# Kernel tuning notes

Hardware: AMD Instinct MI355X
Metric: run time of the kernel (lower is better)

The kernel has to match this reference:

```python
import jax, jax.numpy as jnp
import numpy as np

B, V, E, K, H = 8, 4096, 256, 6, 8
HD = E // H  # head dim = 32


def _knn_idx(x, k):
    # brute-force squared-euclidean KNN (pytorch3d knn_points, return_sorted=True)
    sq = jnp.sum(x * x, axis=-1)                      # [B, V]
    d2 = sq[:, :, None] + sq[:, None, :] - 2.0 * jnp.einsum('bie,bje->bij', x, x)  # [B,V,V]
    _, idx = jax.lax.top_k(-d2, k)                    # ascending distance -> [B, V, K]
    return idx


def setup_inputs() -> dict:
    key = jax.random.key(0)
    kx, kq, kk, kv, ko = jax.random.split(key, 5)
    s = 1.0 / np.sqrt(E)
    return {
        'x':  jax.random.normal(kx, (B, V, E), dtype=jnp.float32),
        'Wq': jax.random.normal(kq, (E, E), dtype=jnp.float32) * s,
        'Wk': jax.random.normal(kk, (E, E), dtype=jnp.float32) * s,
        'Wv': jax.random.normal(kv, (E, E), dtype=jnp.float32) * s,
        'Wo': jax.random.normal(ko, (E, E), dtype=jnp.float32) * s,
    }


def reference(x, Wq, Wk, Wv, Wo):
    idx = _knn_idx(x, K)                                   # [B, V, K] int32
    k = jax.vmap(lambda xb, ib: xb[ib])(x, idx)            # gather -> [B, V, K, E]
    v = k - x[:, :, None, :]                               # use_direction: v = k - q

    # per-point 1-query / K-key multihead attention (bias-free, eval mode)
    scale = 1.0 / np.sqrt(HD)
    qh = (x @ Wq.T).reshape(B, V, H, HD)                   # [B,V,H,HD]
    kh = jnp.einsum('bvke,fe->bvkf', k, Wk).reshape(B, V, K, H, HD)
    vh = jnp.einsum('bvke,fe->bvkf', v, Wv).reshape(B, V, K, H, HD)
    scores = jnp.einsum('bvhd,bvkhd->bvhk', qh, kh) * scale  # [B,V,H,K]
    attn = jax.nn.softmax(scores, axis=-1)
    out = jnp.einsum('bvhk,bvkhd->bvhd', attn, vh).reshape(B, V, E) @ Wo.T

    # attention weights averaged over heads, scatter-added onto neighbor ids
    x_w = jnp.mean(attn, axis=2)                            # [B, V, K]
    x_w = jax.vmap(lambda i, w: jnp.zeros((V,), x.dtype).at[i].add(w))(
        idx.reshape(B, -1), x_w.reshape(B, -1))             # [B, V]

    return x + out, x_w
```

## Files before the change

### kernel.cpp

```cpp
#include <hip/hip_runtime.h>
#include <cfloat>
#include <math.h>

#define B_   8
#define V_   4096
#define E_   256
#define K_   6
#define H_   8
#define HD_  32
#define NPTS (B_*V_)

typedef __bf16 bf16x8 __attribute__((ext_vector_type(8)));
typedef float  f32x4  __attribute__((ext_vector_type(4)));
typedef float  f32x16 __attribute__((ext_vector_type(16)));

__device__ __forceinline__ float bf2f(unsigned short u) {
    return __uint_as_float(((unsigned int)u) << 16);
}
__device__ __forceinline__ unsigned short f2bf(float f) {
    unsigned int u = __float_as_uint(f);
    return (unsigned short)((u + 0x7fffu + ((u >> 16) & 1u)) >> 16);
}
__device__ __forceinline__ unsigned int med3u(unsigned int a, unsigned int b,
                                              unsigned int c) {
    unsigned int d;
    asm("v_med3_u32 %0, %1, %2, %3" : "=v"(d) : "v"(a), "v"(b), "v"(c));
    return d;
}
__device__ __forceinline__ void push6(unsigned int (&k6)[6], unsigned int key) {
    k6[5] = med3u(k6[4], k6[5], key);
    k6[4] = med3u(k6[3], k6[4], key);
    k6[3] = med3u(k6[2], k6[3], key);
    k6[2] = med3u(k6[1], k6[2], key);
    k6[1] = med3u(k6[0], k6[1], key);
    k6[0] = min(k6[0], key);
}
__device__ __forceinline__ unsigned int bfscale2(unsigned int u) {
    return (u + 0x05000500u) ^ 0x80008000u;
}

__global__ __launch_bounds__(256) void cvtsq_kernel(const float* __restrict__ x,
                                                    const float* __restrict__ Wq,
                                                    const float* __restrict__ Wk,
                                                    const float* __restrict__ Wv,
                                                    const float* __restrict__ Wo,
                                                    unsigned short* __restrict__ xh,
                                                    unsigned short* __restrict__ Wh,
                                                    float* __restrict__ sqp,
                                                    float* __restrict__ xw) {
    const int bx = blockIdx.x;
    if (bx < 4096) {
        size_t i = ((size_t)bx * 256 + threadIdx.x) * 8;
        float4 a = *reinterpret_cast<const float4*>(x + i);
        float4 b = *reinterpret_cast<const float4*>(x + i + 4);
        ushort o[8] = { f2bf(a.x), f2bf(a.y), f2bf(a.z), f2bf(a.w),
                        f2bf(b.x), f2bf(b.y), f2bf(b.z), f2bf(b.w) };
        *reinterpret_cast<uint4*>(xh + i) = *reinterpret_cast<uint4*>(o);
        float s = a.x*a.x + a.y*a.y + a.z*a.z + a.w*a.w
                + b.x*b.x + b.y*b.y + b.z*b.z + b.w*b.w;
        s += __shfl_xor(s, 1);
        s += __shfl_xor(s, 2);
        s += __shfl_xor(s, 4);
        s += __shfl_xor(s, 8);
        s += __shfl_xor(s, 16);
        if ((threadIdx.x & 31) == 0) {
            int p = bx * 8 + (threadIdx.x >> 5);
            int b_ = p >> 12, col = p & 4095;
            int stripe = col >> 10, cc = col & 1023;
            int t = cc >> 5, rem = cc & 31;
            int h = (rem >> 2) & 1;
            int reg = (rem & 3) | ((rem >> 3) << 2);
            int i2 = (b_ << 12) | (stripe << 10) | (t << 5) | (h << 4) | reg;
            sqp[i2] = (s + 600.f) * 512.f;
        }
    } else {
        const int wb = bx - 4096;
        xw[wb * 256 + threadIdx.x] = 0.f;
        const int m = wb >> 5;
        const float* src = (m == 0) ? Wq : (m == 1) ? Wk : (m == 2) ? Wv : Wo;
        unsigned short* dst = Wh + (size_t)m * 65536;
        size_t i = ((size_t)(wb & 31) * 256 + threadIdx.x) * 8;
        float4 a = *reinterpret_cast<const float4*>(src + i);
        float4 b = *reinterpret_cast<const float4*>(src + i + 4);
        ushort o[8] = { f2bf(a.x), f2bf(a.y), f2bf(a.z), f2bf(a.w),
                        f2bf(b.x), f2bf(b.y), f2bf(b.z), f2bf(b.w) };
        *reinterpret_cast<uint4*>(dst + i) = *reinterpret_cast<uint4*>(o);
    }
}

__global__ __launch_bounds__(256, 2) void knn13_kernel(const unsigned short* __restrict__ xh,
                                                       const float* __restrict__ sqp,
                                                       unsigned int* __restrict__ cand) {
    __shared__ __align__(16) char smem[36864];

    const int b      = blockIdx.z;
    const int row0   = blockIdx.x * 256;
    const int stripe = blockIdx.y;
    const int colbase = stripe * 1024;
    const int tid = threadIdx.x;
    const int w   = tid >> 6;
    const int l   = tid & 63;
    const int ln  = l & 31;
    const int h   = l >> 5;
    const unsigned short* Xb = xh + ((size_t)b << 12) * E_;

    const int myrow0 = row0 + (w << 6) + ln;
    bf16x8 brow0[16], brow1[16];
#pragma unroll
    for (int kg = 0; kg < 16; ++kg) {
        uint4 u0 = *reinterpret_cast<const uint4*>(
            Xb + ((size_t)myrow0 << 8) + kg * 16 + h * 8);
        uint4 u1 = *reinterpret_cast<const uint4*>(
            Xb + ((size_t)(myrow0 + 32) << 8) + kg * 16 + h * 8);
        u0.x = bfscale2(u0.x); u0.y = bfscale2(u0.y);
        u0.z = bfscale2(u0.z); u0.w = bfscale2(u0.w);
        u1.x = bfscale2(u1.x); u1.y = bfscale2(u1.y);
        u1.z = bfscale2(u1.z); u1.w = bfscale2(u1.w);
        brow0[kg] = *reinterpret_cast<bf16x8*>(&u0);
        brow1[kg] = *reinterpret_cast<bf16x8*>(&u1);
    }

    unsigned int bk0[6], bk1[6];
#pragma unroll
    for (int s = 0; s < 6; ++s) { bk0[s] = 0xFFFFFFFFu; bk1[s] = 0xFFFFFFFFu; }

    __builtin_amdgcn_global_load_lds(
        (const __attribute__((address_space(1))) void*)
            (sqp + ((size_t)(b * 4 + stripe) << 10) + tid * 4),
        (__attribute__((address_space(3))) void*)(smem + 32768 + tid * 16), 16, 0, 0);
#pragma unroll
    for (int it = 0; it < 4; ++it) {
        int li = it * 256 + tid, col = li >> 5, sl = li & 31;
        const unsigned short* gp =
            Xb + ((size_t)(colbase + col) << 8) + ((sl ^ (col & 7)) << 3);
        __builtin_amdgcn_global_load_lds(
            (const __attribute__((address_space(1))) void*)gp,
            (__attribute__((address_space(3))) void*)(smem + li * 16), 16, 0, 0);
    }
    __syncthreads();

    for (int t = 0; t < 32; ++t) {
        const int cur = (t & 1) * 16384;
        if (t < 31) {
            char* nbuf = smem + (cur ^ 16384);
            const int c0n = colbase + (t + 1) * 32;
#pragma unroll
            for (int it = 0; it < 4; ++it) {
                int li = it * 256 + tid, col = li >> 5, sl = li & 31;
                const unsigned short* gp =
                    Xb + ((size_t)(c0n + col) << 8) + ((sl ^ (col & 7)) << 3);
                __builtin_amdgcn_global_load_lds(
                    (const __attribute__((address_space(1))) void*)gp,
                    (__attribute__((address_space(3))) void*)(nbuf + li * 16), 16, 0, 0);
            }
        }
        const char* sb = smem + 32768 + t * 128 + h * 64;
        f32x16 acc0;
#pragma unroll
        for (int q = 0; q < 4; ++q) {
            f32x4 sv = *reinterpret_cast<const f32x4*>(sb + q * 16);
            acc0[q * 4 + 0] = sv[0];
            acc0[q * 4 + 1] = sv[1];
            acc0[q * 4 + 2] = sv[2];
            acc0[q * 4 + 3] = sv[3];
        }
        f32x16 acc1 = acc0;

        const char* abase = smem + cur + ln * 512;
        const int swz = (ln & 7);
#pragma unroll
        for (int kg = 0; kg < 16; ++kg) {
            bf16x8 af = *reinterpret_cast<const bf16x8*>(
                abase + ((((kg << 1) + h) ^ swz) << 4));
            acc0 = __builtin_amdgcn_mfma_f32_32x32x16_bf16(af, brow0[kg], acc0, 0, 0, 0);
            acc1 = __builtin_amdgcn_mfma_f32_32x32x16_bf16(af, brow1[kg], acc1, 0, 0, 0);
        }

        const unsigned int cb0 = (unsigned int)(colbase + (t << 5) + (h << 2));
#pragma unroll
        for (int r = 0; r < 16; ++r) {
            unsigned int cidx = cb0 + (r & 3) + ((r >> 2) << 3);
            push6(bk0, ((unsigned int)acc0[r] << 12) | cidx);
            push6(bk1, ((unsigned int)acc1[r] << 12) | cidx);
        }
        __syncthreads();
    }

    size_t p0 = ((size_t)b << 12) + myrow0;
    unsigned int* op0 = cand + p0 * 48 + stripe * 12 + h * 6;
    unsigned int* op1 = cand + (p0 + 32) * 48 + stripe * 12 + h * 6;
#pragma unroll
    for (int s = 0; s < 6; ++s) { op0[s] = bk0[s]; op1[s] = bk1[s]; }
}

__global__ __launch_bounds__(256) void sel_kernel(const unsigned int* __restrict__ cand,
                                                  unsigned short* __restrict__ c16,
                                                  int* __restrict__ idxout,
                                                  unsigned char* __restrict__ flag) {
    int p = blockIdx.x * 256 + threadIdx.x;
    const unsigned int* cp = cand + (size_t)p * 48;
    unsigned int tk[16];
#pragma unroll
    for (int s = 0; s < 16; ++s) tk[s] = 0xFFFFFFFFu;
    for (int j = 0; j < 48; ++j) {
        unsigned int key = cp[j];
#pragma unroll
        for (int s = 15; s > 0; --s) tk[s] = med3u(tk[s - 1], tk[s], key);
        tk[0] = min(tk[0], key);
    }
    unsigned short* op = c16 + (size_t)p * 16;
#pragma unroll
    for (int s = 0; s < 16; ++s) op[s] = (unsigned short)(tk[s] & 4095u);
    int* ip = idxout + (size_t)p * K_;
#pragma unroll
    for (int s = 0; s < 6; ++s) ip[s] = (int)(tk[s] & 4095u);
    float d6 = (float)(tk[5] >> 12) * 0.001953125f;
    float d7 = (float)(tk[6] >> 12) * 0.001953125f;
    flag[p] = (d7 - d6 < 0.4f) ? 1 : 0;
}

__global__ __launch_bounds__(256) void refine_kernel(const float* __restrict__ x,
                                                     const unsigned short* __restrict__ c16,
                                                     const unsigned char* __restrict__ flag,
                                                     int* __restrict__ idxout) {
    int wv = threadIdx.x >> 6;
    int lane = threadIdx.x & 63;
    const int bid = blockIdx.x;
    const int nbk = ((bid & 7) << 10) | (bid >> 3);
    int p = nbk * 4 + wv;
    if (!flag[p]) return;
    int b = p >> 12;
    int vi = p & 4095;
    const float* Xb = x + ((size_t)b << 12) * E_;
    const int half = lane >> 5;
    const int hl = lane & 31;

    double xi[8];
#pragma unroll
    for (int t = 0; t < 8; ++t) xi[t] = (double)Xb[(size_t)vi * E_ + hl + t * 32];

    double bdist[6]; int bidx[6];
#pragma unroll
    for (int s = 0; s < 6; ++s) { bdist[s] = DBL_MAX; bidx[s] = 0x7fffffff; }

    const unsigned short* cp = c16 + (size_t)p * 16;
    for (int c = 0; c < 16; c += 2) {
        int jme = cp[c + half];
        const float* Xj = Xb + (size_t)jme * E_;
        double s = 0.0;
#pragma unroll
        for (int t = 0; t < 8; ++t) {
            double d = xi[t] - (double)Xj[hl + t * 32];
            s = fma(d, d, s);
        }
#pragma unroll
        for (int off = 16; off; off >>= 1) s += __shfl_xor(s, off);
        double sv[2];
        sv[0] = __shfl(s, 0);
        sv[1] = __shfl(s, 32);
        int jv[2] = { (int)cp[c], (int)cp[c + 1] };
#pragma unroll
        for (int q = 0; q < 2; ++q) {
            double sq_ = sv[q]; int j = jv[q];
            if (sq_ < bdist[5] || (sq_ == bdist[5] && j < bidx[5])) {
                bdist[5] = sq_; bidx[5] = j;
#pragma unroll
                for (int t = 5; t > 0; --t) {
                    if (bdist[t] < bdist[t - 1] ||
                        (bdist[t] == bdist[t - 1] && bidx[t] < bidx[t - 1])) {
                        double td = bdist[t]; bdist[t] = bdist[t - 1]; bdist[t - 1] = td;
                        int    ti = bidx[t];  bidx[t]  = bidx[t - 1];  bidx[t - 1]  = ti;
                    } else break;
                }
            }
        }
    }
    if (lane == 0) {
        int* op = idxout + (size_t)p * K_;
#pragma unroll
        for (int s = 0; s < 6; ++s) op[s] = bidx[s];
    }
}

__global__ __launch_bounds__(256, 2) void proj_mfma(const unsigned short* __restrict__ xh,
                                                    const unsigned short* __restrict__ Wh,
                                                    unsigned short* __restrict__ Y) {
    const int tid = threadIdx.x;
    const int w = tid >> 6, l = tid & 63, cl = l & 15, g = l >> 4;
    const int row0 = blockIdx.x * 128;
    const int wsel = blockIdx.y;
    const unsigned short* W = Wh + (size_t)wsel * 65536;

    bf16x8 a0[8], a1[8];
    const int ar0 = row0 + (w << 4) + cl;
#pragma unroll
    for (int ks = 0; ks < 8; ++ks) {
        a0[ks] = *reinterpret_cast<const bf16x8*>(xh + ((size_t)ar0 << 8) + ks * 32 + g * 8);
        a1[ks] = *reinterpret_cast<const bf16x8*>(xh + ((size_t)(ar0 + 64) << 8) + ks * 32 + g * 8);
    }

    bf16x8 wf[8];
    {
        const unsigned short* Wr = W + (size_t)cl * 256 + g * 8;
#pragma unroll
        for (int ks = 0; ks < 8; ++ks)
            wf[ks] = *reinterpret_cast<const bf16x8*>(Wr + ks * 32);
    }

#pragma unroll
    for (int ct = 0; ct < 16; ++ct) {
        bf16x8 wn[8];
        if (ct < 15) {
            const unsigned short* Wr = W + (size_t)((ct + 1) * 16 + cl) * 256 + g * 8;
#pragma unroll
            for (int ks = 0; ks < 8; ++ks)
                wn[ks] = *reinterpret_cast<const bf16x8*>(Wr + ks * 32);
        }
        f32x4 acc0 = {0.f, 0.f, 0.f, 0.f};
        f32x4 acc1 = {0.f, 0.f, 0.f, 0.f};
#pragma unroll
        for (int ks = 0; ks < 8; ++ks) {
            acc0 = __builtin_amdgcn_mfma_f32_16x16x32_bf16(a0[ks], wf[ks], acc0, 0, 0, 0);
            acc1 = __builtin_amdgcn_mfma_f32_16x16x32_bf16(a1[ks], wf[ks], acc1, 0, 0, 0);
        }
#pragma unroll
        for (int r = 0; r < 4; ++r) {
            size_t row = row0 + (w << 4) + (g << 2) + r;
            Y[row * 768 + wsel * 256 + ct * 16 + cl] = f2bf(acc0[r]);
            Y[(row + 64) * 768 + wsel * 256 + ct * 16 + cl] = f2bf(acc1[r]);
        }
#pragma unroll
        for (int ks = 0; ks < 8; ++ks) wf[ks] = wn[ks];
    }
}

__global__ __launch_bounds__(256) void attn16_kernel(const unsigned short* __restrict__ Y,
                                                     const int* __restrict__ idx,
                                                     const unsigned short* __restrict__ WoH,
                                                     const float* __restrict__ x,
                                                     float* __restrict__ out,
                                                     float* __restrict__ xw) {
    __shared__ __align__(16) unsigned short P[16][264];
    const int bid = blockIdx.x;
    const int blk = ((bid & 7) << 8) | (bid >> 3);
    const int w = threadIdx.x >> 6;
    const int l = threadIdx.x & 63;
    const int p0 = blk * 16;
    const int b = p0 >> 12;
    const size_t bbase = (size_t)(b << 12) * 768;

    for (int j = 0; j < 4; ++j) {
        const int p = p0 + w * 4 + j;
        const int* ip = idx + (size_t)p * K_;
        int nb[K_];
#pragma unroll
        for (int k = 0; k < K_; ++k) nb[k] = ip[k];

        const unsigned short* Yp = Y + (size_t)p * 768;
        ushort4 q4 = *reinterpret_cast<const ushort4*>(Yp + l * 4);
        ushort4 s4 = *reinterpret_cast<const ushort4*>(Yp + 512 + l * 4);
        float q0 = bf2f(q4.x), q1 = bf2f(q4.y), q2 = bf2f(q4.z), q3 = bf2f(q4.w);
        float v0 = bf2f(s4.x), v1 = bf2f(s4.y), v2 = bf2f(s4.z), v3 = bf2f(s4.w);

        float sc[K_];
#pragma unroll
        for (int k = 0; k < K_; ++k) {
            ushort4 k4 = *reinterpret_cast<const ushort4*>(
                Y + bbase + (size_t)nb[k] * 768 + 256 + l * 4);
            float s = q0 * bf2f(k4.x) + q1 * bf2f(k4.y)
                    + q2 * bf2f(k4.z) + q3 * bf2f(k4.w);
            s += __shfl_xor(s, 1);
            s += __shfl_xor(s, 2);
            s += __shfl_xor(s, 4);
            sc[k] = s * 0.17677669529663687f;
        }
        float m = sc[0];
#pragma unroll
        for (int k = 1; k < K_; ++k) m = fmaxf(m, sc[k]);
        float e[K_], sum = 0.f;
#pragma unroll
        for (int k = 0; k < K_; ++k) { e[k] = __expf(sc[k] - m); sum += e[k]; }
        float inv = 1.f / sum;

        float o0 = 0.f, o1 = 0.f, o2 = 0.f, o3 = 0.f;
        float hs[K_];
#pragma unroll
        for (int k = 0; k < K_; ++k) {
            float a = e[k] * inv;
            ushort4 z4 = *reinterpret_cast<const ushort4*>(
                Y + bbase + (size_t)nb[k] * 768 + 512 + l * 4);
            o0 += a * (bf2f(z4.x) - v0);
            o1 += a * (bf2f(z4.y) - v1);
            o2 += a * (bf2f(z4.z) - v2);
            o3 += a * (bf2f(z4.w) - v3);
            float t = a;
            t += __shfl_xor(t, 8);
            t += __shfl_xor(t, 16);
            t += __shfl_xor(t, 32);
            hs[k] = t * 0.125f;
        }
        ushort o4[4] = { f2bf(o0), f2bf(o1), f2bf(o2), f2bf(o3) };
        *reinterpret_cast<ushort4*>(&P[w * 4 + j][l * 4]) =
            *reinterpret_cast<ushort4*>(o4);
        if (l < K_) atomicAdd(&xw[(b << 12) + nb[l]], hs[l]);
    }
    __syncthreads();

    const int cl = l & 15, g = l >> 4;
    bf16x8 a[8];
#pragma unroll
    for (int ks = 0; ks < 8; ++ks)
        a[ks] = *reinterpret_cast<const bf16x8*>(&P[cl][ks * 32 + g * 8]);

#pragma unroll
    for (int ct = 0; ct < 4; ++ct) {
        const int col0 = w * 64 + ct * 16;
        f32x4 acc = {0.f, 0.f, 0.f, 0.f};
        const unsigned short* Wr = WoH + (size_t)(col0 + cl) * 256 + g * 8;
#pragma unroll
        for (int ks = 0; ks < 8; ++ks) {
            bf16x8 bf = *reinterpret_cast<const bf16x8*>(Wr + ks * 32);
            acc = __builtin_amdgcn_mfma_f32_16x16x32_bf16(a[ks], bf, acc, 0, 0, 0);
        }
#pragma unroll
        for (int r = 0; r < 4; ++r) {
            size_t o = (size_t)(p0 + (g << 2) + r) * E_ + col0 + cl;
            out[o] = acc[r] + x[o];
        }
    }
}

extern "C" void kernel_launch(void* const* d_in, const int* in_sizes, int n_in,
                              void* d_out, int out_size, void* d_ws, size_t ws_size,
                              hipStream_t stream) {
    const float* x  = (const float*)d_in[0];
    const float* Wq = (const float*)d_in[1];
    const float* Wk = (const float*)d_in[2];
    const float* Wv = (const float*)d_in[3];
    const float* Wo = (const float*)d_in[4];

    float* out = (float*)d_out;
    float* xw  = out + (size_t)NPTS * E_;

    char* ws = (char*)d_ws;
    float*          sqpw  = (float*)(ws + 131072);
    unsigned int*   candw = (unsigned int*)(ws + 262144);
    int*            idxw  = (int*)(ws + 6553600);
    unsigned char*  flagw = (unsigned char*)(ws + 7340032);
    unsigned short* Wh    = (unsigned short*)(ws + 7372800);
    unsigned short* c16w  = (unsigned short*)(ws + 7897088);
    unsigned short* Xh    = (unsigned short*)(ws + 8945664);
    unsigned short* Y     = (unsigned short*)(ws + 25722880);

    cvtsq_kernel<<<4096 + 128, 256, 0, stream>>>(x, Wq, Wk, Wv, Wo, Xh, Wh, sqpw, xw);
    knn13_kernel<<<dim3(V_ / 256, 4, B_), 256, 0, stream>>>(Xh, sqpw, candw);
    sel_kernel<<<NPTS / 256, 256, 0, stream>>>(candw, c16w, idxw, flagw);
    refine_kernel<<<NPTS / 4, 256, 0, stream>>>(x, c16w, flagw, idxw);
    proj_mfma<<<dim3(NPTS / 128, 3), 256, 0, stream>>>(Xh, Wh, Y);
    attn16_kernel<<<NPTS / 16, 256, 0, stream>>>(Y, idxw, Wh + 3 * 65536, x, out, xw);
}
```

Baseline: 229.3 us.

## Stage projection weight tiles in LDS via async global_load_lds double buffering

Each wave previously loaded its own copy of the weight tile straight from global memory into registers, so the four waves in a block fetched the same data redundantly. The weights are now loaded once per block into a swizzled, double-buffered LDS tile of 32 output columns using direct global-to-LDS loads, and each wave reads its fragments from LDS. The intent is to cut global and L2 traffic and register pressure in the projection GEMM. In exchange it adds 32KB of LDS per block and a barrier per tile step, which may limit occupancy and serialise the pipeline.

```diff
diff --git a/kernel.cpp b/kernel.cpp
--- a/kernel.cpp
+++ b/kernel.cpp
@@ -285,6 +285,7 @@
 __global__ __launch_bounds__(256, 2) void proj_mfma(const unsigned short* __restrict__ xh,
                                                     const unsigned short* __restrict__ Wh,
                                                     unsigned short* __restrict__ Y) {
+    __shared__ __align__(16) char smem[32768];
     const int tid = threadIdx.x;
     const int w = tid >> 6, l = tid & 63, cl = l & 15, g = l >> 4;
     const int row0 = blockIdx.x * 128;
@@ -299,38 +300,54 @@
         a1[ks] = *reinterpret_cast<const bf16x8*>(xh + ((size_t)(ar0 + 64) << 8) + ks * 32 + g * 8);
     }
 
-    bf16x8 wf[8];
-    {
-        const unsigned short* Wr = W + (size_t)cl * 256 + g * 8;
-#pragma unroll
-        for (int ks = 0; ks < 8; ++ks)
-            wf[ks] = *reinterpret_cast<const bf16x8*>(Wr + ks * 32);
-    }
-
-#pragma unroll
-    for (int ct = 0; ct < 16; ++ct) {
-        bf16x8 wn[8];
-        if (ct < 15) {
-            const unsigned short* Wr = W + (size_t)((ct + 1) * 16 + cl) * 256 + g * 8;
-#pragma unroll
-            for (int ks = 0; ks < 8; ++ks)
-                wn[ks] = *reinterpret_cast<const bf16x8*>(Wr + ks * 32);
-        }
-        f32x4 acc0 = {0.f, 0.f, 0.f, 0.f};
-        f32x4 acc1 = {0.f, 0.f, 0.f, 0.f};
-#pragma unroll
-        for (int ks = 0; ks < 8; ++ks) {
-            acc0 = __builtin_amdgcn_mfma_f32_16x16x32_bf16(a0[ks], wf[ks], acc0, 0, 0, 0);
-            acc1 = __builtin_amdgcn_mfma_f32_16x16x32_bf16(a1[ks], wf[ks], acc1, 0, 0, 0);
-        }
-#pragma unroll
-        for (int r = 0; r < 4; ++r) {
-            size_t row = row0 + (w << 4) + (g << 2) + r;
-            Y[row * 768 + wsel * 256 + ct * 16 + cl] = f2bf(acc0[r]);
-            Y[(row + 64) * 768 + wsel * 256 + ct * 16 + cl] = f2bf(acc1[r]);
-        }
-#pragma unroll
-        for (int ks = 0; ks < 8; ++ks) wf[ks] = wn[ks];
+#pragma unroll
+    for (int it = 0; it < 4; ++it) {
+        int li = it * 256 + tid, col = li >> 5, sl = li & 31;
+        const unsigned short* gp = W + ((size_t)col << 8) + ((sl ^ (col & 7)) << 3);
+        __builtin_amdgcn_global_load_lds(
+            (const __attribute__((address_space(1))) void*)gp,
+            (__attribute__((address_space(3))) void*)(smem + li * 16), 16, 0, 0);
+    }
+    __syncthreads();
+
+    for (int tp = 0; tp < 8; ++tp) {
+        const int cur = (tp & 1) * 16384;
+        if (tp < 7) {
+            char* nbuf = smem + (cur ^ 16384);
+            const int colb = (tp + 1) * 32;
+#pragma unroll
+            for (int it = 0; it < 4; ++it) {
+                int li = it * 256 + tid, col = li >> 5, sl = li & 31;
+                const unsigned short* gp =
+                    W + ((size_t)(colb + col) << 8) + ((sl ^ (col & 7)) << 3);
+                __builtin_amdgcn_global_load_lds(
+                    (const __attribute__((address_space(1))) void*)gp,
+                    (__attribute__((address_space(3))) void*)(nbuf + li * 16), 16, 0, 0);
+            }
+        }
+#pragma unroll
+        for (int c01 = 0; c01 < 2; ++c01) {
+            const int ct = tp * 2 + c01;
+            const int wr = c01 * 16 + cl;
+            const char* wbase = smem + cur + wr * 512;
+            const int swz = wr & 7;
+            f32x4 acc0 = {0.f, 0.f, 0.f, 0.f};
+            f32x4 acc1 = {0.f, 0.f, 0.f, 0.f};
+#pragma unroll
+            for (int ks = 0; ks < 8; ++ks) {
+                bf16x8 wf = *reinterpret_cast<const bf16x8*>(
+                    wbase + ((((ks << 2) + g) ^ swz) << 4));
+                acc0 = __builtin_amdgcn_mfma_f32_16x16x32_bf16(a0[ks], wf, acc0, 0, 0, 0);
+                acc1 = __builtin_amdgcn_mfma_f32_16x16x32_bf16(a1[ks], wf, acc1, 0, 0, 0);
+            }
+#pragma unroll
+            for (int r = 0; r < 4; ++r) {
+                size_t row = row0 + (w << 4) + (g << 2) + r;
+                Y[row * 768 + wsel * 256 + ct * 16 + cl] = f2bf(acc0[r]);
+                Y[(row + 64) * 768 + wsel * 256 + ct * 16 + cl] = f2bf(acc1[r]);
+            }
+        }
+        __syncthreads();
     }
 }
 
```

New measurement: 195.3 us. -14.8%, faster.
